# Performance work log

Measured on AMD Instinct MI355X. Metric: run time of the kernel, lower is better.

The kernel has to match this reference:

```python
import jax, jax.numpy as jnp
import numpy as np

V, E, H, K, B, T = 50000, 128, 256, 9, 128, 512
HD = H // 2  # hidden per direction


def setup_inputs() -> dict:
    key = jax.random.key(0)
    ks = jax.random.split(key, 16)
    s = 0.1
    inp = {
        "x": jax.random.randint(ks[0], (B, T), 0, V),
        "emb": jax.random.normal(ks[1], (V, E), jnp.float32) * 0.02,
        "w_ih_f": jax.random.normal(ks[2], (4 * HD, E), jnp.float32) * s,
        "w_hh_f": jax.random.normal(ks[3], (4 * HD, HD), jnp.float32) * s,
        "b_ih_f": jax.random.normal(ks[4], (4 * HD,), jnp.float32) * s,
        "b_hh_f": jax.random.normal(ks[5], (4 * HD,), jnp.float32) * s,
        "w_ih_b": jax.random.normal(ks[6], (4 * HD, E), jnp.float32) * s,
        "w_hh_b": jax.random.normal(ks[7], (4 * HD, HD), jnp.float32) * s,
        "b_ih_b": jax.random.normal(ks[8], (4 * HD,), jnp.float32) * s,
        "b_hh_b": jax.random.normal(ks[9], (4 * HD,), jnp.float32) * s,
        "W_tag": jax.random.normal(ks[10], (K, H), jnp.float32) * s,
        "b_tag": jax.random.normal(ks[11], (K,), jnp.float32) * s,
        "start_trans": jax.random.normal(ks[12], (K,), jnp.float32) * s,
        "end_trans": jax.random.normal(ks[13], (K,), jnp.float32) * s,
        "trans": jax.random.normal(ks[14], (K, K), jnp.float32) * s,
    }
    return inp


def _lstm_dir(xs, w_ih, w_hh, b_ih, b_hh, reverse):
    # xs: [T, B, E]; PyTorch gate order: i, f, g, o
    Bsz = xs.shape[1]
    hd = w_hh.shape[1]
    b = b_ih + b_hh

    def step(carry, x_t):
        h, c = carry
        gates = x_t @ w_ih.T + h @ w_hh.T + b  # [B, 4*hd]
        i, f, g, o = jnp.split(gates, 4, axis=-1)
        i = jax.nn.sigmoid(i)
        f = jax.nn.sigmoid(f)
        g = jnp.tanh(g)
        o = jax.nn.sigmoid(o)
        c = f * c + i * g
        h = o * jnp.tanh(c)
        return (h, c), h

    init = (jnp.zeros((Bsz, hd), xs.dtype), jnp.zeros((Bsz, hd), xs.dtype))
    _, hs = jax.lax.scan(step, init, xs, reverse=reverse)
    return hs  # [T, B, hd], time-ordered


def _viterbi(emissions, start_trans, end_trans, trans):
    # emissions: [T, B, K]; returns best tag path [B, T] (torchcrf decode, no mask)
    score0 = start_trans[None, :] + emissions[0]  # [B, K]

    def step(score, emis_t):
        # score[b, i] + trans[i, j] -> best over i
        cand = score[:, :, None] + trans[None, :, :]  # [B, K, K]
        bp = jnp.argmax(cand, axis=1)                 # [B, K] best prev tag
        best = jnp.max(cand, axis=1)
        return best + emis_t, bp

    final_score, bps = jax.lax.scan(step, score0, emissions[1:])  # bps: [T-1, B, K]
    final_score = final_score + end_trans[None, :]
    last_tag = jnp.argmax(final_score, axis=-1)  # [B]

    def back(tag, bp):
        prev = jnp.take_along_axis(bp, tag[:, None], axis=1)[:, 0]
        return prev, prev

    _, path = jax.lax.scan(back, last_tag, bps, reverse=True)  # [T-1, B]
    tags = jnp.concatenate([path, last_tag[None, :]], axis=0)  # [T, B]
    return tags.T.astype(jnp.int32)  # [B, T]


def reference(x, emb, w_ih_f, w_hh_f, b_ih_f, b_hh_f,
              w_ih_b, w_hh_b, b_ih_b, b_hh_b,
              W_tag, b_tag, start_trans, end_trans, trans):
    xt = x.T                        # [T, B]
    e = emb[xt]                     # [T, B, E] embedding gather
    h_f = _lstm_dir(e, w_ih_f, w_hh_f, b_ih_f, b_hh_f, reverse=False)
    h_b = _lstm_dir(e, w_ih_b, w_hh_b, b_ih_b, b_hh_b, reverse=True)
    h = jnp.concatenate([h_f, h_b], axis=-1)  # [T, B, H]
    # dropout is identity at inference
    emissions = h @ W_tag.T + b_tag           # [T, B, K]
    return _viterbi(emissions, start_trans, end_trans, trans)
```

## Files before the change

### kernel.cpp

```cpp
#include <hip/hip_runtime.h>
#include <math.h>

#define TT 512
#define BB 128
#define KK 9

__device__ __forceinline__ float fast_sigmoid(float x) {
    const float LOG2E = 1.4426950408889634f;
    float e = __builtin_amdgcn_exp2f(-x * LOG2E);
    return __builtin_amdgcn_rcpf(1.0f + e);
}
__device__ __forceinline__ float fast_tanh(float x) {
    const float LOG2E = 1.4426950408889634f;
    float a = fabsf(x);
    float e = __builtin_amdgcn_exp2f(-2.0f * a * LOG2E);
    float t = (1.0f - e) * __builtin_amdgcn_rcpf(1.0f + e);
    return copysignf(t, x);
}

__global__ __launch_bounds__(256, 1) void input_gemm(
    const int* __restrict__ x, const float* __restrict__ emb,
    const float* __restrict__ w_ih_f, const float* __restrict__ w_ih_b,
    const float* __restrict__ b_ih_f, const float* __restrict__ b_hh_f,
    const float* __restrict__ b_ih_b, const float* __restrict__ b_hh_b,
    float* __restrict__ buf_f, float* __restrict__ buf_b,
    int t0f, int t0b)
{
    const int dir = blockIdx.z;
    const int s   = blockIdx.x;
    const int n0  = blockIdx.y * 128;
    const int t   = (dir ? t0b : t0f) + s;
    const float* w  = dir ? w_ih_b : w_ih_f;
    const float* bi = dir ? b_ih_b : b_ih_f;
    const float* bh = dir ? b_hh_b : b_hh_f;
    float* dst = dir ? buf_b : buf_f;

    __shared__ __align__(16) float As[128][136];
    __shared__ __align__(16) float Bs[128][136];
    __shared__ int tok_s[128];

    const int tid  = threadIdx.x;
    const int rsub = tid >> 5;
    const int koff = (tid & 31) * 4;

    if (tid < 128) tok_s[tid] = x[tid * TT + t];
    __syncthreads();

    #pragma unroll
    for (int it = 0; it < 16; it++) {
        const int row = it * 8 + rsub;
        const int swz = (it & 7) * 4;
        const float4 av = *(const float4*)(emb + (size_t)tok_s[row] * 128 + koff);
        const float4 bv = *(const float4*)(w + (size_t)(n0 + row) * 128 + koff);
        *(float4*)&As[row][koff ^ swz] = av;
        *(float4*)&Bs[row][koff ^ swz] = bv;
    }
    __syncthreads();

    const int tx = tid & 15;
    const int ty = tid >> 4;

    float acc[8][8];
    #pragma unroll
    for (int i = 0; i < 8; i++)
        #pragma unroll
        for (int j = 0; j < 8; j++) acc[i][j] = 0.0f;

    const int swzA = (ty & 7) * 4;
    const int swzB = (tx & 7) * 4;

    #pragma unroll 4
    for (int k4 = 0; k4 < 32; k4++) {
        const int kA = (k4 * 4) ^ swzA;
        const int kB = (k4 * 4) ^ swzB;
        float4 a4[8], b4[8];
        #pragma unroll
        for (int i = 0; i < 8; i++) a4[i] = *(const float4*)&As[ty * 8 + i][kA];
        #pragma unroll
        for (int j = 0; j < 8; j++) b4[j] = *(const float4*)&Bs[tx * 8 + j][kB];
        #pragma unroll
        for (int i = 0; i < 8; i++)
            #pragma unroll
            for (int j = 0; j < 8; j++)
                acc[i][j] += a4[i].x * b4[j].x + a4[i].y * b4[j].y
                           + a4[i].z * b4[j].z + a4[i].w * b4[j].w;
    }

    const int nbase = n0 + tx * 8;
    float bias[8];
    #pragma unroll
    for (int j = 0; j < 8; j++) {
        int n = nbase + j;
        bias[j] = bi[n] + bh[n];
    }
    #pragma unroll
    for (int i = 0; i < 8; i++) {
        int brow = ty * 8 + i;
        float* o = dst + ((size_t)s * 128 + brow) * 512 + nbase;
        float4 v0, v1;
        v0.x = acc[i][0] + bias[0]; v0.y = acc[i][1] + bias[1];
        v0.z = acc[i][2] + bias[2]; v0.w = acc[i][3] + bias[3];
        v1.x = acc[i][4] + bias[4]; v1.y = acc[i][5] + bias[5];
        v1.z = acc[i][6] + bias[6]; v1.w = acc[i][7] + bias[7];
        *(float4*)o = v0;
        *(float4*)(o + 4) = v1;
    }
}

__global__ __launch_bounds__(512, 2) void lstm_chunk(
    const float* __restrict__ buf_f, const float* __restrict__ buf_b,
    const float* __restrict__ w_hh_f, const float* __restrict__ w_hh_b,
    float* __restrict__ h_all,
    float* __restrict__ h_state, float* __restrict__ c_state,
    int t0f, int t0b, int C, int init)
{
    const int dir = blockIdx.x >> 7;
    const int b   = blockIdx.x & 127;
    const int j   = threadIdx.x;
    const int w_  = j >> 6;
    const int l   = j & 63;
    const int m   = l >> 2;
    const int q   = l & 3;
    const int k   = w_ * 16 + m;
    const int r   = q * 128 + k;

    const float* whh = dir ? w_hh_b : w_hh_f;
    float wR[128];
    #pragma unroll
    for (int qq = 0; qq < 32; qq++) {
        float4 v = *(const float4*)(whh + (size_t)r * 128 + qq * 4);
        wR[4*qq+0] = v.x; wR[4*qq+1] = v.y; wR[4*qq+2] = v.z; wR[4*qq+3] = v.w;
    }

    __shared__ __align__(16) float h_lds[2][128];
    float c;
    if (init) {
        c = 0.0f;
        if (q == 0) h_lds[0][k] = 0.0f;
    } else {
        c = c_state[((size_t)dir * 128 + b) * 128 + k];
        if (q == 0) h_lds[0][k] = h_state[((size_t)dir * 128 + b) * 128 + k];
    }
    __syncthreads();

    const float* buf = dir ? buf_b : buf_f;
    const int t0     = dir ? t0b : t0f;
    const int  tl0   = dir ? (C - 1) : 0;
    const long lstep = dir ? -(long)(128 * 512) : (long)(128 * 512);

    const float* xp = buf + ((size_t)tl0 * 128 + b) * 512 + r;
    float xw = *xp;
    float h_reg = 0.0f;

    for (int s = 0; s < C; s++) {
        const int t = t0 + (dir ? (C - 1 - s) : s);
        const int p = s & 1;
        const float* hprev = h_lds[p];

        float a0 = 0.f, a1 = 0.f, a2 = 0.f, a3 = 0.f;
        #pragma unroll
        for (int qq = 0; qq < 32; qq++) {
            float4 h4 = *(const float4*)&hprev[4 * qq];
            a0 += wR[4*qq+0] * h4.x;
            a1 += wR[4*qq+1] * h4.y;
            a2 += wR[4*qq+2] * h4.z;
            a3 += wR[4*qq+3] * h4.w;
        }
        float pre = xw + ((a0 + a1) + (a2 + a3));

        float act = (q == 2) ? fast_tanh(pre) : fast_sigmoid(pre);

        float f_ = __shfl_xor(act, 1);
        float g_ = __shfl_xor(act, 2);
        float o_ = __shfl_xor(act, 3);

        c = f_ * c + act * g_;
        h_reg = o_ * fast_tanh(c);
        if (q == 0) h_lds[p ^ 1][k] = h_reg;

        __syncthreads();

        if (s + 1 < C) { xp += lstep; xw = *xp; }
        if (q == 0)
            h_all[((size_t)t * BB + b) * 256 + dir * 128 + k] = h_reg;
    }

    if (q == 0) {
        h_state[((size_t)dir * 128 + b) * 128 + k] = h_reg;
        c_state[((size_t)dir * 128 + b) * 128 + k] = c;
    }
}

__global__ __launch_bounds__(256) void emis_kernel(
    const float* __restrict__ h_all, const float* __restrict__ W_tag,
    const float* __restrict__ b_tag, float* __restrict__ em_sum)
{
    const int wid  = threadIdx.x >> 6;
    const int lane = threadIdx.x & 63;
    const size_t m = (size_t)blockIdx.x * 4 + wid;
    const float4 hv = *(const float4*)(h_all + m * 256 + lane * 4);
    #pragma unroll
    for (int kk = 0; kk < KK; kk++) {
        const float4 wv = *(const float4*)(W_tag + kk * 256 + lane * 4);
        float p = hv.x * wv.x + hv.y * wv.y + hv.z * wv.z + hv.w * wv.w;
        #pragma unroll
        for (int off = 32; off > 0; off >>= 1) p += __shfl_down(p, off);
        if (lane == 0) em_sum[m * KK + kk] = p + b_tag[kk];
    }
}

__device__ __forceinline__ void vmax(float va, int ia, float vb, int ib,
                                     float& vo, int& io) {
    bool gt = vb > va;
    vo = gt ? vb : va;
    io = gt ? ib : ia;
}

__global__ __launch_bounds__(64) void viterbi_kernel(
    const float* __restrict__ em_sum,
    const float* __restrict__ start_trans, const float* __restrict__ end_trans,
    const float* __restrict__ trans, int* __restrict__ out)
{
    const int b = blockIdx.x;
    const int lane = threadIdx.x;
    __shared__ float em_s[TT * KK];
    __shared__ unsigned char bp[TT][KK];

    for (int f = lane; f < TT * KK; f += 64) {
        int t = f / KK, kk = f - t * KK;
        em_s[f] = em_sum[((size_t)t * BB + b) * KK + kk];
    }
    __syncthreads();

    float trans_col[KK];
    float score = -1e30f;
    if (lane < KK) {
        #pragma unroll
        for (int i = 0; i < KK; i++) trans_col[i] = trans[i * KK + lane];
        score = start_trans[lane] + em_s[lane];
    }

    for (int t = 1; t < TT; t++) {
        float my = (lane < KK) ? score : -1e30f;
        float cand[KK];
        #pragma unroll
        for (int i = 0; i < KK; i++) cand[i] = __shfl(my, i) + trans_col[i];

        float v01, v23, v45, v67, v03, v47, v07, vb_;
        int   i01, i23, i45, i67, i03, i47, i07, ib_;
        vmax(cand[0], 0, cand[1], 1, v01, i01);
        vmax(cand[2], 2, cand[3], 3, v23, i23);
        vmax(cand[4], 4, cand[5], 5, v45, i45);
        vmax(cand[6], 6, cand[7], 7, v67, i67);
        vmax(v01, i01, v23, i23, v03, i03);
        vmax(v45, i45, v67, i67, v47, i47);
        vmax(v03, i03, v47, i47, v07, i07);
        vmax(v07, i07, cand[8], 8, vb_, ib_);

        if (lane < KK) {
            bp[t][lane] = (unsigned char)ib_;
            score = vb_ + em_s[t * KK + lane];
        }
    }

    float fin = (lane < KK) ? (score + end_trans[lane]) : -1e30f;
    float farr[KK];
    #pragma unroll
    for (int jx = 0; jx < KK; jx++) farr[jx] = __shfl(fin, jx);
    float v01, v23, v45, v67, v03, v47, v07, vb_;
    int   i01, i23, i45, i67, i03, i47, i07, bj;
    vmax(farr[0], 0, farr[1], 1, v01, i01);
    vmax(farr[2], 2, farr[3], 3, v23, i23);
    vmax(farr[4], 4, farr[5], 5, v45, i45);
    vmax(farr[6], 6, farr[7], 7, v67, i67);
    vmax(v01, i01, v23, i23, v03, i03);
    vmax(v45, i45, v67, i67, v47, i47);
    vmax(v03, i03, v47, i47, v07, i07);
    vmax(v07, i07, farr[8], 8, vb_, bj);

    if (lane == 0) {
        int tag = bj;
        out[b * TT + (TT - 1)] = tag;
        for (int t = TT - 1; t >= 1; t--) {
            tag = bp[t][tag];
            out[b * TT + t - 1] = tag;
        }
    }
}

extern "C" void kernel_launch(void* const* d_in, const int* in_sizes, int n_in,
                              void* d_out, int out_size, void* d_ws, size_t ws_size,
                              hipStream_t stream)
{
    const int*   x       = (const int*)  d_in[0];
    const float* emb     = (const float*)d_in[1];
    const float* w_ih_f  = (const float*)d_in[2];
    const float* w_hh_f  = (const float*)d_in[3];
    const float* b_ih_f  = (const float*)d_in[4];
    const float* b_hh_f  = (const float*)d_in[5];
    const float* w_ih_b  = (const float*)d_in[6];
    const float* w_hh_b  = (const float*)d_in[7];
    const float* b_ih_b  = (const float*)d_in[8];
    const float* b_hh_b  = (const float*)d_in[9];
    const float* W_tag   = (const float*)d_in[10];
    const float* b_tag   = (const float*)d_in[11];
    const float* start_t = (const float*)d_in[12];
    const float* end_t   = (const float*)d_in[13];
    const float* trans   = (const float*)d_in[14];
    int* out = (int*)d_out;

    const size_t hall_elems  = (size_t)TT * BB * 256;
    const size_t em_elems    = (size_t)TT * BB * KK;
    const size_t state_elems = (size_t)2 * 128 * 128;

    int C = 32;
    const int cands[5] = {512, 256, 128, 64, 32};
    for (int ci = 0; ci < 5; ci++) {
        size_t need = ((size_t)2 * cands[ci] * BB * 512
                       + hall_elems + em_elems
                       + 2 * state_elems) * sizeof(float);
        if (ws_size >= need) { C = cands[ci]; break; }
    }

    float* buf_f   = (float*)d_ws;
    float* buf_b   = buf_f + (size_t)C * BB * 512;
    float* em_sum  = buf_b + (size_t)C * BB * 512;
    float* h_state = em_sum + em_elems;
    float* c_state = h_state + state_elems;
    float* h_all   = c_state + state_elems;

    const int rounds = TT / C;
    for (int r = 0; r < rounds; r++) {
        const int t0f = r * C;
        const int t0b = TT - (r + 1) * C;
        dim3 gg(C, 4, 2);
        input_gemm<<<gg, dim3(256), 0, stream>>>(
            x, emb, w_ih_f, w_ih_b, b_ih_f, b_hh_f, b_ih_b, b_hh_b,
            buf_f, buf_b, t0f, t0b);
        lstm_chunk<<<dim3(256), dim3(512), 0, stream>>>(
            buf_f, buf_b, w_hh_f, w_hh_b, h_all,
            h_state, c_state, t0f, t0b, C, (r == 0) ? 1 : 0);
    }
    emis_kernel<<<dim3((TT * BB) / 4), dim3(256), 0, stream>>>(
        h_all, W_tag, b_tag, em_sum);
    viterbi_kernel<<<dim3(BB), dim3(64), 0, stream>>>(
        em_sum, start_t, end_t, trans, out);
}
```

Baseline: 1.056 ms.

## Restructure input GEMM with k-chunked register prefetch, prefetch Viterbi emissions, cap chunk size

```diff
diff --git a/kernel.cpp b/kernel.cpp
--- a/kernel.cpp
+++ b/kernel.cpp
@@ -18,7 +18,7 @@
     return copysignf(t, x);
 }
 
-__global__ __launch_bounds__(256, 1) void input_gemm(
+__global__ __launch_bounds__(256, 3) void input_gemm(
     const int* __restrict__ x, const float* __restrict__ emb,
     const float* __restrict__ w_ih_f, const float* __restrict__ w_ih_b,
     const float* __restrict__ b_ih_f, const float* __restrict__ b_hh_f,
@@ -35,27 +35,16 @@
     const float* bh = dir ? b_hh_b : b_hh_f;
     float* dst = dir ? buf_b : buf_f;
 
-    __shared__ __align__(16) float As[128][136];
-    __shared__ __align__(16) float Bs[128][136];
-    __shared__ int tok_s[128];
+    __shared__ __align__(16) float As[32][132];
+    __shared__ __align__(16) float Bs[32][132];
 
     const int tid  = threadIdx.x;
-    const int rsub = tid >> 5;
-    const int koff = (tid & 31) * 4;
-
-    if (tid < 128) tok_s[tid] = x[tid * TT + t];
-    __syncthreads();
-
-    #pragma unroll
-    for (int it = 0; it < 16; it++) {
-        const int row = it * 8 + rsub;
-        const int swz = (it & 7) * 4;
-        const float4 av = *(const float4*)(emb + (size_t)tok_s[row] * 128 + koff);
-        const float4 bv = *(const float4*)(w + (size_t)(n0 + row) * 128 + koff);
-        *(float4*)&As[row][koff ^ swz] = av;
-        *(float4*)&Bs[row][koff ^ swz] = bv;
-    }
-    __syncthreads();
+    const int lrow = tid >> 3;
+    const int k4   = (tid & 7) * 4;
+
+    int tokr[4];
+    #pragma unroll
+    for (int p = 0; p < 4; p++) tokr[p] = x[(p * 32 + lrow) * TT + t];
 
     const int tx = tid & 15;
     const int ty = tid >> 4;
@@ -66,24 +55,45 @@
         #pragma unroll
         for (int j = 0; j < 8; j++) acc[i][j] = 0.0f;
 
-    const int swzA = (ty & 7) * 4;
-    const int swzB = (tx & 7) * 4;
-
-    #pragma unroll 4
-    for (int k4 = 0; k4 < 32; k4++) {
-        const int kA = (k4 * 4) ^ swzA;
-        const int kB = (k4 * 4) ^ swzB;
-        float4 a4[8], b4[8];
-        #pragma unroll
-        for (int i = 0; i < 8; i++) a4[i] = *(const float4*)&As[ty * 8 + i][kA];
-        #pragma unroll
-        for (int j = 0; j < 8; j++) b4[j] = *(const float4*)&Bs[tx * 8 + j][kB];
-        #pragma unroll
-        for (int i = 0; i < 8; i++)
+    float4 aS[4], bS[4];
+    #pragma unroll
+    for (int p = 0; p < 4; p++) {
+        aS[p] = *(const float4*)(emb + (size_t)tokr[p] * 128 + k4);
+        bS[p] = *(const float4*)(w + (size_t)(n0 + p * 32 + lrow) * 128 + k4);
+    }
+
+    for (int kc = 0; kc < 128; kc += 32) {
+        __syncthreads();
+        #pragma unroll
+        for (int p = 0; p < 4; p++) {
+            const int row = p * 32 + lrow;
+            As[k4 + 0][row] = aS[p].x; As[k4 + 1][row] = aS[p].y;
+            As[k4 + 2][row] = aS[p].z; As[k4 + 3][row] = aS[p].w;
+            Bs[k4 + 0][row] = bS[p].x; Bs[k4 + 1][row] = bS[p].y;
+            Bs[k4 + 2][row] = bS[p].z; Bs[k4 + 3][row] = bS[p].w;
+        }
+        __syncthreads();
+        if (kc + 32 < 128) {
             #pragma unroll
-            for (int j = 0; j < 8; j++)
-                acc[i][j] += a4[i].x * b4[j].x + a4[i].y * b4[j].y
-                           + a4[i].z * b4[j].z + a4[i].w * b4[j].w;
+            for (int p = 0; p < 4; p++) {
+                aS[p] = *(const float4*)(emb + (size_t)tokr[p] * 128 + kc + 32 + k4);
+                bS[p] = *(const float4*)(w + (size_t)(n0 + p * 32 + lrow) * 128 + kc + 32 + k4);
+            }
+        }
+        #pragma unroll 8
+        for (int k = 0; k < 32; k++) {
+            float4 af0 = *(const float4*)&As[k][ty * 8];
+            float4 af1 = *(const float4*)&As[k][ty * 8 + 4];
+            float4 bf0 = *(const float4*)&Bs[k][tx * 8];
+            float4 bf1 = *(const float4*)&Bs[k][tx * 8 + 4];
+            float a_[8] = {af0.x, af0.y, af0.z, af0.w, af1.x, af1.y, af1.z, af1.w};
+            float b_[8] = {bf0.x, bf0.y, bf0.z, bf0.w, bf1.x, bf1.y, bf1.z, bf1.w};
+            #pragma unroll
+            for (int i = 0; i < 8; i++)
+                #pragma unroll
+                for (int j = 0; j < 8; j++)
+                    acc[i][j] += a_[i] * b_[j];
+        }
     }
 
     const int nbase = n0 + tx * 8;
@@ -240,7 +250,10 @@
         score = start_trans[lane] + em_s[lane];
     }
 
+    float em_cur = (lane < KK) ? em_s[KK + lane] : 0.0f;
     for (int t = 1; t < TT; t++) {
+        float em_next = (t + 1 < TT && lane < KK) ? em_s[(t + 1) * KK + lane] : 0.0f;
+
         float my = (lane < KK) ? score : -1e30f;
         float cand[KK];
         #pragma unroll
@@ -259,8 +272,9 @@
 
         if (lane < KK) {
             bp[t][lane] = (unsigned char)ib_;
-            score = vb_ + em_s[t * KK + lane];
-        }
+            score = vb_ + em_cur;
+        }
+        em_cur = em_next;
     }
 
     float fin = (lane < KK) ? (score + end_trans[lane]) : -1e30f;
@@ -314,8 +328,8 @@
     const size_t state_elems = (size_t)2 * 128 * 128;
 
     int C = 32;
-    const int cands[5] = {512, 256, 128, 64, 32};
-    for (int ci = 0; ci < 5; ci++) {
+    const int cands[3] = {128, 64, 32};
+    for (int ci = 0; ci < 3; ci++) {
         size_t need = ((size_t)2 * cands[ci] * BB * 512
                        + hall_elems + em_elems
                        + 2 * state_elems) * sizeof(float);
```

Measured after the change: 953.9 us. 9.7% less time.
